# Performance work log

Hardware: AMD Instinct MI355X
Metric: run time of the kernel (lower is better)

The kernel has to match this reference:

```python
import jax, jax.numpy as jnp
import numpy as np

TEMPERATURE = 0.07  # from init_kwargs
B, N, D = 256, 200000, 128


def setup_inputs() -> dict:
    key = jax.random.key(0)
    k1, k2, k3, k4, k5 = jax.random.split(key, 5)
    codes = jax.random.normal(k1, (B, D), dtype=jnp.float32)
    # Memory bank holds L2-normalized codes (update_memory stores normalized data)
    bank = jax.random.normal(k2, (N, D), dtype=jnp.float32)
    bank = bank / jnp.linalg.norm(bank, axis=1, keepdims=True)
    # background neighbours: ~51 nearest neighbours per sample (sparse mask)
    mask_bg = jax.random.uniform(k3, (B, N)) < (51.0 / N)
    # close-grouper cluster mates: ~N/number_of_centroids members per cluster
    mask_close = jax.random.uniform(k4, (B, N)) < (N / 100 / N)
    # guarantee self index present in both (include_self_index=True semantics)
    self_idx = jax.random.randint(k5, (B,), 0, N)
    rows = jnp.arange(B)
    mask_bg = mask_bg.at[rows, self_idx].set(True)
    mask_int = (mask_bg & mask_close).at[rows, self_idx].set(True)
    return {"codes": codes, "bank": bank, "mask_bg": mask_bg, "mask_int": mask_int}


def reference(codes, bank, mask_bg, mask_int):
    # v = F.normalize(codes, p=2, dim=1)
    v = codes / jnp.linalg.norm(codes, axis=1, keepdims=True)  # [B, D]
    # _prob_density: masked gather from bank, dot with code, exp(./T), sum.
    # Dense-equivalent: full dot matrix once, masked reductions for d1 and d2.
    dots = jnp.einsum("bd,nd->bn", v, bank) / TEMPERATURE  # [B, N]
    e = jnp.exp(dots)
    d1 = jnp.sum(jnp.where(mask_bg, e, 0.0), axis=1)   # background density
    d2 = jnp.sum(jnp.where(mask_int, e, 0.0), axis=1)  # intersect density
    loss = jnp.sum(jnp.log(d1) - jnp.log(d2)) / codes.shape[0]
    return loss
```

## Files before the change

kernel.cpp:

```cpp
#include <hip/hip_runtime.h>
#include <math.h>

#define BB 256
#define NN 200000
#define DD 128
#define INV_T 14.285714285714286f
#define CAP 3072
#define FLUSH_AT (CAP - 2048)

#define WS_FLAG 0
#define WS_D1   64
#define WS_D2   320

__global__ __launch_bounds__(64) void la_zero(unsigned* __restrict__ wsu) {
    const unsigned t = threadIdx.x;
    if (t == 0) wsu[WS_FLAG] = 0u;
    float* wsf = (float*)wsu;
    for (unsigned i = t; i < 512; i += 64) wsf[WS_D1 + i] = 0.f;
}

__global__ __launch_bounds__(256) void la_detect(const unsigned* __restrict__ mbg_w,
                                                 unsigned* __restrict__ wsu) {
    const unsigned g = blockIdx.x * 256u + threadIdx.x;
    int any = 0;
    for (unsigned i = g; i < 50000u; i += 16384u) any |= (mbg_w[i] > 1u) ? 1 : 0;
    if (any) atomicOr((int*)wsu + WS_FLAG, 1);
}

__device__ __forceinline__ void process_hits(const float* __restrict__ bank,
                                             const void* __restrict__ mint_v,
                                             const unsigned* __restrict__ s_ent,
                                             int cnt, int flag, int b,
                                             const float2* __restrict__ code2,
                                             float scale, unsigned lane,
                                             unsigned wid, float& l1, float& l2) {
    for (int i = (int)wid; i < cnt; i += 4) {
        const unsigned n = s_ent[i];
        const float2 cv = code2[lane];
        const float2 bv = ((const float2*)bank)[(size_t)n * 64u + lane];
        float d = fmaf(cv.x, bv.x, cv.y * bv.y);
#pragma unroll
        for (int off = 32; off > 0; off >>= 1) d += __shfl_down(d, off, 64);
        if (lane == 0) {
            const float e = __expf(d * scale);
            l1 += e;
            const unsigned im = (flag == 0)
                ? ((const unsigned*)mint_v)[(size_t)b * NN + n]
                : (unsigned)((const unsigned char*)mint_v)[(size_t)b * NN + n];
            if (im) l2 += e;
        }
    }
}

__global__ __launch_bounds__(256) void la_fused(const float* __restrict__ codes,
                                                const float* __restrict__ bank,
                                                const void* __restrict__ mbg_v,
                                                const void* __restrict__ mint_v,
                                                unsigned* __restrict__ wsu) {
    __shared__ __align__(16) float code_s[DD];
    __shared__ unsigned s_ent[CAP];
    __shared__ unsigned s_cnt;
    __shared__ float s_red[8];
    __shared__ float s_scale;

    const int t = threadIdx.x;
    const unsigned lane = (unsigned)(t & 63);
    const unsigned wid = (unsigned)(t >> 6);
    const int s = blockIdx.x;
    const int b = blockIdx.y;
    const int flag = (int)((volatile unsigned*)wsu)[WS_FLAG];

    if (t == 0) s_cnt = 0u;
    float c = (t < DD) ? codes[b * DD + t] : 0.f;
    if (t < DD) code_s[t] = c;
    float sq = c * c;
#pragma unroll
    for (int off = 32; off > 0; off >>= 1) sq += __shfl_down(sq, off, 64);
    if (lane == 0) s_red[wid] = sq;
    __syncthreads();
    if (t == 0) s_scale = rsqrtf(s_red[0] + s_red[1] + s_red[2] + s_red[3]) * INV_T;
    __syncthreads();
    const float scale = s_scale;
    const float2* code2 = (const float2*)code_s;

    float l1 = 0.f, l2 = 0.f;

    if (flag == 0) {
        const uint4* row = (const uint4*)((const char*)mbg_v + (size_t)b * (NN * 4)) + s * 6250;
        const int n_base = s * 25000;
        for (int it = 0; it < 13; ++it) {
            const int idx0 = it * 512 + t;
            uint4 v[2];
#pragma unroll
            for (int k = 0; k < 2; ++k) {
                const int idx = idx0 + k * 256;
                v[k] = make_uint4(0u, 0u, 0u, 0u);
                if (idx < 6250) v[k] = row[idx];
            }
#pragma unroll
            for (int k = 0; k < 2; ++k) {
                const unsigned gw[4] = {v[k].x, v[k].y, v[k].z, v[k].w};
                const int idx = idx0 + k * 256;
#pragma unroll
                for (int j = 0; j < 4; ++j) {
                    if (gw[j] != 0u) {
                        unsigned pos = atomicAdd(&s_cnt, 1u);
                        if (pos < CAP) s_ent[pos] = (unsigned)(n_base + idx * 4 + j);
                    }
                }
            }
            __syncthreads();
            const int cnt = (int)s_cnt;
            if (cnt >= FLUSH_AT) {
                process_hits(bank, mint_v, s_ent, cnt, flag, b, code2, scale,
                             lane, wid, l1, l2);
                __syncthreads();
                if (t == 0) s_cnt = 0u;
                __syncthreads();
            }
        }
    } else {
        const uint4* rowb = (const uint4*)((const char*)mbg_v + (size_t)b * NN);
        const int w0 = s * 1563;
        const int wend = (s == 7) ? 12500 : (w0 + 1563);
        for (int it = 0; it < 13; ++it) {
            const int idx = w0 + it * 128 + t;
            uint4 v = make_uint4(0u, 0u, 0u, 0u);
            if (t < 128 && idx < wend) v = rowb[idx];
            const unsigned gw[4] = {v.x, v.y, v.z, v.w};
#pragma unroll
            for (int j = 0; j < 16; ++j) {
                if (((gw[j >> 2] >> ((j & 3) * 8)) & 0xffu) != 0u) {
                    unsigned pos = atomicAdd(&s_cnt, 1u);
                    if (pos < CAP) s_ent[pos] = (unsigned)(idx * 16 + j);
                }
            }
            __syncthreads();
            const int cnt = (int)s_cnt;
            if (cnt >= FLUSH_AT) {
                process_hits(bank, mint_v, s_ent, cnt, flag, b, code2, scale,
                             lane, wid, l1, l2);
                __syncthreads();
                if (t == 0) s_cnt = 0u;
                __syncthreads();
            }
        }
    }

    __syncthreads();
    int cnt = (int)s_cnt;
    if (cnt > CAP) cnt = CAP;
    process_hits(bank, mint_v, s_ent, cnt, flag, b, code2, scale, lane, wid, l1, l2);

#pragma unroll
    for (int off = 32; off > 0; off >>= 1) {
        l1 += __shfl_down(l1, off, 64);
        l2 += __shfl_down(l2, off, 64);
    }
    __syncthreads();
    if (lane == 0) { s_red[wid] = l1; s_red[4 + wid] = l2; }
    __syncthreads();
    if (t == 0) {
        float* wsf = (float*)wsu;
        atomicAdd(&wsf[WS_D1 + b], s_red[0] + s_red[1] + s_red[2] + s_red[3]);
        atomicAdd(&wsf[WS_D2 + b], s_red[4] + s_red[5] + s_red[6] + s_red[7]);
    }
}

__global__ __launch_bounds__(256) void la_final(const float* __restrict__ d1,
                                                const float* __restrict__ d2,
                                                float* __restrict__ out) {
    __shared__ float red[4];
    const int t = threadIdx.x;
    float v = logf(d1[t]) - logf(d2[t]);
#pragma unroll
    for (int off = 32; off > 0; off >>= 1) v += __shfl_down(v, off, 64);
    if ((t & 63) == 0) red[t >> 6] = v;
    __syncthreads();
    if (t == 0) out[0] = (red[0] + red[1] + red[2] + red[3]) / (float)BB;
}

extern "C" void kernel_launch(void* const* d_in, const int* in_sizes, int n_in,
                              void* d_out, int out_size, void* d_ws, size_t ws_size,
                              hipStream_t stream) {
    const float* codes = (const float*)d_in[0];
    const float* bank  = (const float*)d_in[1];
    const void*  mbg   = d_in[2];
    const void*  mit   = d_in[3];

    unsigned* wsu = (unsigned*)d_ws;
    float*    wsf = (float*)d_ws;

    la_zero<<<1, 64, 0, stream>>>(wsu);
    la_detect<<<64, 256, 0, stream>>>((const unsigned*)mbg, wsu);
    la_fused<<<dim3(8, BB), 256, 0, stream>>>(codes, bank, mbg, mit, wsu);
    la_final<<<1, 256, 0, stream>>>(wsf + WS_D1, wsf + WS_D2, (float*)d_out);
}
```

Baseline: 409.7 us.

## Use per-wave hit lists, precompute scales, and drop atomics and block barriers

Merges the zero and detect kernels into one init kernel that also precomputes each row's normalization scale and a per-row dtype vote. The fused kernel now gives each wavefront its own shared hit buffer, so it skips block-wide barriers during the scan and skips empty chunks with a wave-level any. The byte-mask path now loads narrower uint2 words with better coalescing. Partial sums are written per block instead of through float atomics, which removes the need to zero the workspace. In exchange, per-wave buffers are smaller and each wave processes its own hits serially, so load balance can suffer.

Result: no change. 408.7 us, median of 2 (-0.2%).

```diff
diff --git a/kernel.cpp b/kernel.cpp
--- a/kernel.cpp
+++ b/kernel.cpp
@@ -5,48 +5,61 @@
 #define NN 200000
 #define DD 128
 #define INV_T 14.285714285714286f
-#define CAP 3072
-#define FLUSH_AT (CAP - 2048)
-
-#define WS_FLAG 0
-#define WS_D1   64
-#define WS_D2   320
-
-__global__ __launch_bounds__(64) void la_zero(unsigned* __restrict__ wsu) {
-    const unsigned t = threadIdx.x;
-    if (t == 0) wsu[WS_FLAG] = 0u;
-    float* wsf = (float*)wsu;
-    for (unsigned i = t; i < 512; i += 64) wsf[WS_D1 + i] = 0.f;
-}
-
-__global__ __launch_bounds__(256) void la_detect(const unsigned* __restrict__ mbg_w,
-                                                 unsigned* __restrict__ wsu) {
-    const unsigned g = blockIdx.x * 256u + threadIdx.x;
-    int any = 0;
-    for (unsigned i = g; i < 50000u; i += 16384u) any |= (mbg_w[i] > 1u) ? 1 : 0;
-    if (any) atomicOr((int*)wsu + WS_FLAG, 1);
-}
-
-__device__ __forceinline__ void process_hits(const float* __restrict__ bank,
-                                             const void* __restrict__ mint_v,
-                                             const unsigned* __restrict__ s_ent,
+
+#define CAPW 768
+#define FLUSHW (CAPW - 512)
+
+#define WS_VOTE  0
+#define WS_SCALE 256
+#define WS_P1    512
+#define WS_P2    2560
+
+__global__ __launch_bounds__(256) void la_init(const float* __restrict__ codes,
+                                               const unsigned* __restrict__ mbg_w,
+                                               unsigned* __restrict__ wsu) {
+    __shared__ float s_red[4];
+    __shared__ unsigned s_any[4];
+    const int t = threadIdx.x;
+    const unsigned lane = (unsigned)(t & 63);
+    const unsigned wid = (unsigned)(t >> 6);
+    const int b = blockIdx.x;
+
+    const unsigned i = (unsigned)(b * 256 + t);
+    const int any = (i < 50000u) && (mbg_w[i] > 1u);
+    const unsigned long long bal = __ballot(any);
+    if (lane == 0) s_any[wid] = (bal != 0ull) ? 1u : 0u;
+
+    float c = (t < DD) ? codes[b * DD + t] : 0.f;
+    float sq = c * c;
+#pragma unroll
+    for (int off = 32; off > 0; off >>= 1) sq += __shfl_down(sq, off, 64);
+    if (lane == 0) s_red[wid] = sq;
+    __syncthreads();
+    if (t == 0) {
+        float* wsf = (float*)wsu;
+        wsf[WS_SCALE + b] = rsqrtf(s_red[0] + s_red[1] + s_red[2] + s_red[3]) * INV_T;
+        wsu[WS_VOTE + b] = s_any[0] | s_any[1] | s_any[2] | s_any[3];
+    }
+}
+
+__device__ __forceinline__ void process_wave(const float2* __restrict__ bank2,
+                                             const unsigned* __restrict__ m32,
+                                             const unsigned char* __restrict__ m8,
+                                             const unsigned* __restrict__ ent,
                                              int cnt, int flag, int b,
-                                             const float2* __restrict__ code2,
-                                             float scale, unsigned lane,
-                                             unsigned wid, float& l1, float& l2) {
-    for (int i = (int)wid; i < cnt; i += 4) {
-        const unsigned n = s_ent[i];
-        const float2 cv = code2[lane];
-        const float2 bv = ((const float2*)bank)[(size_t)n * 64u + lane];
+                                             float2 cv, float scale,
+                                             unsigned lane, float& l1, float& l2) {
+    for (int i = 0; i < cnt; ++i) {
+        const unsigned n = ent[i];
+        const float2 bv = bank2[(size_t)n * 64u + lane];
+        const unsigned im = (flag == 0) ? m32[(size_t)b * NN + n]
+                                        : (unsigned)m8[(size_t)b * NN + n];
         float d = fmaf(cv.x, bv.x, cv.y * bv.y);
 #pragma unroll
         for (int off = 32; off > 0; off >>= 1) d += __shfl_down(d, off, 64);
         if (lane == 0) {
             const float e = __expf(d * scale);
             l1 += e;
-            const unsigned im = (flag == 0)
-                ? ((const unsigned*)mint_v)[(size_t)b * NN + n]
-                : (unsigned)((const unsigned char*)mint_v)[(size_t)b * NN + n];
             if (im) l2 += e;
         }
     }
@@ -57,122 +70,118 @@
                                                 const void* __restrict__ mbg_v,
                                                 const void* __restrict__ mint_v,
                                                 unsigned* __restrict__ wsu) {
-    __shared__ __align__(16) float code_s[DD];
-    __shared__ unsigned s_ent[CAP];
-    __shared__ unsigned s_cnt;
+    __shared__ unsigned s_ent[4][CAPW];
+    __shared__ unsigned s_cnt[4];
     __shared__ float s_red[8];
-    __shared__ float s_scale;
 
     const int t = threadIdx.x;
     const unsigned lane = (unsigned)(t & 63);
     const unsigned wid = (unsigned)(t >> 6);
     const int s = blockIdx.x;
     const int b = blockIdx.y;
-    const int flag = (int)((volatile unsigned*)wsu)[WS_FLAG];
-
-    if (t == 0) s_cnt = 0u;
-    float c = (t < DD) ? codes[b * DD + t] : 0.f;
-    if (t < DD) code_s[t] = c;
-    float sq = c * c;
-#pragma unroll
-    for (int off = 32; off > 0; off >>= 1) sq += __shfl_down(sq, off, 64);
-    if (lane == 0) s_red[wid] = sq;
-    __syncthreads();
-    if (t == 0) s_scale = rsqrtf(s_red[0] + s_red[1] + s_red[2] + s_red[3]) * INV_T;
-    __syncthreads();
-    const float scale = s_scale;
-    const float2* code2 = (const float2*)code_s;
+
+    const unsigned v4 = wsu[WS_VOTE + lane] | wsu[WS_VOTE + 64 + lane] |
+                        wsu[WS_VOTE + 128 + lane] | wsu[WS_VOTE + 192 + lane];
+    const int flag = (__ballot(v4 != 0u) != 0ull) ? 1 : 0;
+
+    if (lane == 0) s_cnt[wid] = 0u;
+    const float scale = ((const float*)wsu)[WS_SCALE + b];
+    const float2 cv = ((const float2*)codes)[b * 64 + (int)lane];
+    const float2* bank2 = (const float2*)bank;
+    const unsigned* m32 = (const unsigned*)mint_v;
+    const unsigned char* m8 = (const unsigned char*)mint_v;
+    unsigned* ent = s_ent[wid];
+    const int n_base = s * 25000;
 
     float l1 = 0.f, l2 = 0.f;
 
     if (flag == 0) {
-        const uint4* row = (const uint4*)((const char*)mbg_v + (size_t)b * (NN * 4)) + s * 6250;
-        const int n_base = s * 25000;
+        const uint4* row = (const uint4*)((const char*)mbg_v + (size_t)b * ((size_t)NN * 4)) + s * 6250;
         for (int it = 0; it < 13; ++it) {
-            const int idx0 = it * 512 + t;
-            uint4 v[2];
-#pragma unroll
-            for (int k = 0; k < 2; ++k) {
-                const int idx = idx0 + k * 256;
-                v[k] = make_uint4(0u, 0u, 0u, 0u);
-                if (idx < 6250) v[k] = row[idx];
-            }
-#pragma unroll
-            for (int k = 0; k < 2; ++k) {
-                const unsigned gw[4] = {v[k].x, v[k].y, v[k].z, v[k].w};
-                const int idx = idx0 + k * 256;
-#pragma unroll
-                for (int j = 0; j < 4; ++j) {
-                    if (gw[j] != 0u) {
-                        unsigned pos = atomicAdd(&s_cnt, 1u);
-                        if (pos < CAP) s_ent[pos] = (unsigned)(n_base + idx * 4 + j);
-                    }
-                }
-            }
-            __syncthreads();
-            const int cnt = (int)s_cnt;
-            if (cnt >= FLUSH_AT) {
-                process_hits(bank, mint_v, s_ent, cnt, flag, b, code2, scale,
-                             lane, wid, l1, l2);
-                __syncthreads();
-                if (t == 0) s_cnt = 0u;
-                __syncthreads();
+            const int i0 = it * 512 + t;
+            const int i1 = i0 + 256;
+            uint4 v0 = make_uint4(0u, 0u, 0u, 0u), v1 = make_uint4(0u, 0u, 0u, 0u);
+            if (i0 < 6250) v0 = row[i0];
+            if (i1 < 6250) v1 = row[i1];
+            const bool h0 = (v0.x | v0.y | v0.z | v0.w) != 0u;
+            const bool h1 = (v1.x | v1.y | v1.z | v1.w) != 0u;
+            if (__any((int)(h0 | h1))) {
+                if (h0) {
+                    const unsigned gw[4] = {v0.x, v0.y, v0.z, v0.w};
+#pragma unroll
+                    for (int j = 0; j < 4; ++j)
+                        if (gw[j] != 0u) {
+                            const unsigned pos = atomicAdd(&s_cnt[wid], 1u);
+                            if (pos < CAPW) ent[pos] = (unsigned)(n_base + i0 * 4 + j);
+                        }
+                }
+                if (h1) {
+                    const unsigned gw[4] = {v1.x, v1.y, v1.z, v1.w};
+#pragma unroll
+                    for (int j = 0; j < 4; ++j)
+                        if (gw[j] != 0u) {
+                            const unsigned pos = atomicAdd(&s_cnt[wid], 1u);
+                            if (pos < CAPW) ent[pos] = (unsigned)(n_base + i1 * 4 + j);
+                        }
+                }
+                const int cnt = (int)*(volatile unsigned*)&s_cnt[wid];
+                if (cnt >= FLUSHW) {
+                    process_wave(bank2, m32, m8, ent, cnt, flag, b, cv, scale, lane, l1, l2);
+                    if (lane == 0) s_cnt[wid] = 0u;
+                }
             }
         }
     } else {
-        const uint4* rowb = (const uint4*)((const char*)mbg_v + (size_t)b * NN);
-        const int w0 = s * 1563;
-        const int wend = (s == 7) ? 12500 : (w0 + 1563);
+        const uint2* row2 = (const uint2*)((const char*)mbg_v + (size_t)b * NN) + s * 3125;
         for (int it = 0; it < 13; ++it) {
-            const int idx = w0 + it * 128 + t;
-            uint4 v = make_uint4(0u, 0u, 0u, 0u);
-            if (t < 128 && idx < wend) v = rowb[idx];
-            const unsigned gw[4] = {v.x, v.y, v.z, v.w};
-#pragma unroll
-            for (int j = 0; j < 16; ++j) {
-                if (((gw[j >> 2] >> ((j & 3) * 8)) & 0xffu) != 0u) {
-                    unsigned pos = atomicAdd(&s_cnt, 1u);
-                    if (pos < CAP) s_ent[pos] = (unsigned)(idx * 16 + j);
-                }
-            }
-            __syncthreads();
-            const int cnt = (int)s_cnt;
-            if (cnt >= FLUSH_AT) {
-                process_hits(bank, mint_v, s_ent, cnt, flag, b, code2, scale,
-                             lane, wid, l1, l2);
-                __syncthreads();
-                if (t == 0) s_cnt = 0u;
-                __syncthreads();
+            const int i0 = it * 256 + t;
+            uint2 v = make_uint2(0u, 0u);
+            if (i0 < 3125) v = row2[i0];
+            const bool h = (v.x | v.y) != 0u;
+            if (__any((int)h)) {
+                if (h) {
+                    const unsigned gw[2] = {v.x, v.y};
+#pragma unroll
+                    for (int j = 0; j < 8; ++j)
+                        if (((gw[j >> 2] >> ((j & 3) * 8)) & 0xffu) != 0u) {
+                            const unsigned pos = atomicAdd(&s_cnt[wid], 1u);
+                            if (pos < CAPW) ent[pos] = (unsigned)(n_base + i0 * 8 + j);
+                        }
+                }
+                const int cnt = (int)*(volatile unsigned*)&s_cnt[wid];
+                if (cnt >= FLUSHW) {
+                    process_wave(bank2, m32, m8, ent, cnt, flag, b, cv, scale, lane, l1, l2);
+                    if (lane == 0) s_cnt[wid] = 0u;
+                }
             }
         }
     }
 
-    __syncthreads();
-    int cnt = (int)s_cnt;
-    if (cnt > CAP) cnt = CAP;
-    process_hits(bank, mint_v, s_ent, cnt, flag, b, code2, scale, lane, wid, l1, l2);
-
-#pragma unroll
-    for (int off = 32; off > 0; off >>= 1) {
-        l1 += __shfl_down(l1, off, 64);
-        l2 += __shfl_down(l2, off, 64);
-    }
-    __syncthreads();
+    int cnt = (int)*(volatile unsigned*)&s_cnt[wid];
+    if (cnt > CAPW) cnt = CAPW;
+    process_wave(bank2, m32, m8, ent, cnt, flag, b, cv, scale, lane, l1, l2);
+
     if (lane == 0) { s_red[wid] = l1; s_red[4 + wid] = l2; }
     __syncthreads();
     if (t == 0) {
         float* wsf = (float*)wsu;
-        atomicAdd(&wsf[WS_D1 + b], s_red[0] + s_red[1] + s_red[2] + s_red[3]);
-        atomicAdd(&wsf[WS_D2 + b], s_red[4] + s_red[5] + s_red[6] + s_red[7]);
-    }
-}
-
-__global__ __launch_bounds__(256) void la_final(const float* __restrict__ d1,
-                                                const float* __restrict__ d2,
+        wsf[WS_P1 + b * 8 + s] = s_red[0] + s_red[1] + s_red[2] + s_red[3];
+        wsf[WS_P2 + b * 8 + s] = s_red[4] + s_red[5] + s_red[6] + s_red[7];
+    }
+}
+
+__global__ __launch_bounds__(256) void la_final(const unsigned* __restrict__ wsu,
                                                 float* __restrict__ out) {
     __shared__ float red[4];
     const int t = threadIdx.x;
-    float v = logf(d1[t]) - logf(d2[t]);
+    const float* wsf = (const float*)wsu;
+    float s1 = 0.f, s2 = 0.f;
+#pragma unroll
+    for (int s = 0; s < 8; ++s) {
+        s1 += wsf[WS_P1 + t * 8 + s];
+        s2 += wsf[WS_P2 + t * 8 + s];
+    }
+    float v = logf(s1) - logf(s2);
 #pragma unroll
     for (int off = 32; off > 0; off >>= 1) v += __shfl_down(v, off, 64);
     if ((t & 63) == 0) red[t >> 6] = v;
@@ -189,10 +198,8 @@
     const void*  mit   = d_in[3];
 
     unsigned* wsu = (unsigned*)d_ws;
-    float*    wsf = (float*)d_ws;
-
-    la_zero<<<1, 64, 0, stream>>>(wsu);
-    la_detect<<<64, 256, 0, stream>>>((const unsigned*)mbg, wsu);
+
+    la_init<<<BB, 256, 0, stream>>>(codes, (const unsigned*)mbg, wsu);
     la_fused<<<dim3(8, BB), 256, 0, stream>>>(codes, bank, mbg, mit, wsu);
-    la_final<<<1, 256, 0, stream>>>(wsf + WS_D1, wsf + WS_D2, (float*)d_out);
-}
+    la_final<<<1, 256, 0, stream>>>(wsu, (float*)d_out);
+}
```
